# Performance work log

Hardware: AMD Instinct MI355X
Metric: run time of the kernel (lower is better)

Reference implementation:

```python
import jax, jax.numpy as jnp
import numpy as np

N = 100000
D = 128
E = 600000


def setup_inputs() -> dict:
    key = jax.random.key(0)
    k = jax.random.split(key, 7)
    x = jax.random.normal(k[0], (N, D), dtype=jnp.float32)
    edge_index = jax.random.randint(k[1], (2, E), 0, N, dtype=jnp.int32)
    edge_weight = jax.random.uniform(k[2], (E,), dtype=jnp.float32)
    # Linear params (torch nn.Linear: y = x @ W.T + b), init scale ~ 1/sqrt(D)
    s = 1.0 / np.sqrt(D)
    W1 = jax.random.uniform(k[3], (D, D), minval=-s, maxval=s, dtype=jnp.float32)
    b1 = jax.random.uniform(k[4], (D,), minval=-s, maxval=s, dtype=jnp.float32)
    W2 = jax.random.uniform(k[5], (D, D), minval=-s, maxval=s, dtype=jnp.float32)
    b2 = jax.random.uniform(k[6], (D,), minval=-s, maxval=s, dtype=jnp.float32)
    return {"x": x, "edge_index": edge_index, "edge_weight": edge_weight,
            "W1": W1, "b1": b1, "W2": W2, "b2": b2}


def reference(x, edge_index, edge_weight, W1, b1, W2, b2):
    row, col = edge_index[0], edge_index[1]
    # gather-weight-scatter: agg[col] += w * x[row]
    msgs = edge_weight[:, None] * x[row]            # [E, D]
    agg = jax.ops.segment_sum(msgs, col, num_segments=x.shape[0])  # [N, D]
    h = (agg + x) @ W1.T + b1 + (agg * x) @ W2.T + b2
    out = jax.nn.leaky_relu(h, negative_slope=0.2)
    # dropout omitted (eval-mode reference)
    return out
```

## Files before the change

### kernel.cpp

```cpp
#include <hip/hip_runtime.h>

#define D 128

typedef __attribute__((ext_vector_type(8))) short short8;
typedef __attribute__((ext_vector_type(4))) float f32x4;

struct OvfE { int dst, row; float w; };

__device__ __forceinline__ unsigned int f2bf(float f) {
  unsigned int u = __float_as_uint(f);
  return (u + 0x7fffu + ((u >> 16) & 1u)) >> 16;
}

__global__ __launch_bounds__(256) void pre_k(
    const float* __restrict__ x, unsigned short* __restrict__ xbf, int n8, int XB,
    const int* __restrict__ ei, const float* __restrict__ ew,
    int* __restrict__ deg, int* __restrict__ ovfcnt,
    int2* __restrict__ slots, OvfE* __restrict__ ovf, int ovfcap,
    int capLog2, int E, int FB,
    const float* __restrict__ W1, const float* __restrict__ b1,
    const float* __restrict__ W2, const float* __restrict__ b2,
    unsigned short* __restrict__ Bpack, float* __restrict__ bsum) {
  int b = blockIdx.x;
  if (b < XB) {
    int tid = b * 256 + threadIdx.x;
    if (tid >= n8) return;
    float4 a = ((const float4*)x)[(size_t)tid * 2];
    float4 c = ((const float4*)x)[(size_t)tid * 2 + 1];
    uint4 o;
    o.x = f2bf(a.x) | (f2bf(a.y) << 16);
    o.y = f2bf(a.z) | (f2bf(a.w) << 16);
    o.z = f2bf(c.x) | (f2bf(c.y) << 16);
    o.w = f2bf(c.z) | (f2bf(c.w) << 16);
    ((uint4*)xbf)[tid] = o;
  } else if (b < XB + FB) {
    int e = (b - XB) * 256 + threadIdx.x;
    if (e >= E) return;
    int c = ei[E + e];
    int p = atomicAdd(&deg[c], 1);
    if (p < (1 << capLog2)) {
      slots[((size_t)c << capLog2) + p] = make_int2(ei[e], __float_as_int(ew[e]));
    } else {
      int oi = atomicAdd(ovfcnt, 1);
      if (oi < ovfcap) { ovf[oi].dst = c; ovf[oi].row = ei[e]; ovf[oi].w = ew[e]; }
    }
  } else {
    int tid = (b - XB - FB) * 256 + threadIdx.x;
    if (tid < 32768) {
      int j = tid & 7;
      int l = (tid >> 3) & 63;
      int ktnt = tid >> 9;
      int kt = ktnt >> 3, nt = ktnt & 7;
      int k = kt * 32 + ((l >> 4) << 3) + j;
      int col = nt * 16 + (l & 15);
      float v = (k < 128) ? W1[col * 128 + k] : W2[col * 128 + (k - 128)];
      Bpack[tid] = (unsigned short)f2bf(v);
    }
    if (tid < 128) bsum[tid] = b1[tid] + b2[tid];
  }
}

__global__ __launch_bounds__(256, 4) void aggfused_k(
    const unsigned short* __restrict__ xbf, const float* __restrict__ x,
    const int* __restrict__ deg, const int2* __restrict__ slots,
    const int* __restrict__ ovfcnt, const OvfE* __restrict__ ovf,
    const unsigned short* __restrict__ Bpack, const float* __restrict__ bsum,
    float* __restrict__ out, int Nn, int capLog2, int usebf) {
  constexpr int ROWB = 528;
  __shared__ __align__(16) unsigned char Us[64 * ROWB];
  const int t = threadIdx.x;
  const int node0 = blockIdx.x * 64;
  const int lane = t & 63, w = t >> 6;
  const int half = lane >> 5, sl = lane & 31;
  const int cap = 1 << capLog2;

  int dall = 0;
  {
    int g = node0 + w * 16 + lane;
    if (lane < 16 && g < Nn) dall = deg[g];
  }
  int ovn = 0;
  if (__any(dall > cap)) ovn = *ovfcnt;

  for (int ii = 0; ii < 8; ++ii) {
    int nodeIdx = ii * 2 + half;
    int g = node0 + w * 16 + nodeIdx;
    int dv = __shfl(dall, nodeIdx);
    f32x4 acc = {0.f, 0.f, 0.f, 0.f};
    if (g < Nn && dv > 0) {
      int d = min(dv, cap);
      const int2* sb = slots + ((size_t)g << capLog2);
      if (usebf) {
        for (int p = 0; p < d; p += 8) {
          int2 e[8];
          #pragma unroll
          for (int q = 0; q < 8; ++q) e[q] = sb[min(p + q, d - 1)];
          uint2 v[8];
          #pragma unroll
          for (int q = 0; q < 8; ++q)
            v[q] = *(const uint2*)(xbf + (size_t)e[q].x * D + sl * 4);
          #pragma unroll
          for (int q = 0; q < 8; ++q) {
            float wt = (p + q < d) ? __int_as_float(e[q].y) : 0.f;
            acc[0] += wt * __uint_as_float(v[q].x << 16);
            acc[1] += wt * __uint_as_float(v[q].x & 0xffff0000u);
            acc[2] += wt * __uint_as_float(v[q].y << 16);
            acc[3] += wt * __uint_as_float(v[q].y & 0xffff0000u);
          }
        }
      } else {
        for (int p = 0; p < d; p += 8) {
          int2 e[8];
          #pragma unroll
          for (int q = 0; q < 8; ++q) e[q] = sb[min(p + q, d - 1)];
          float4 v[8];
          #pragma unroll
          for (int q = 0; q < 8; ++q)
            v[q] = ((const float4*)(x + (size_t)e[q].x * D))[sl];
          #pragma unroll
          for (int q = 0; q < 8; ++q) {
            float wt = (p + q < d) ? __int_as_float(e[q].y) : 0.f;
            acc[0] += wt * v[q].x;
            acc[1] += wt * v[q].y;
            acc[2] += wt * v[q].z;
            acc[3] += wt * v[q].w;
          }
        }
      }
      if (dv > cap) {
        for (int j = 0; j < ovn; ++j) {
          if (ovf[j].dst == g) {
            float wt = ovf[j].w;
            int r = ovf[j].row;
            if (usebf) {
              uint2 v = *(const uint2*)(xbf + (size_t)r * D + sl * 4);
              acc[0] += wt * __uint_as_float(v.x << 16);
              acc[1] += wt * __uint_as_float(v.x & 0xffff0000u);
              acc[2] += wt * __uint_as_float(v.y << 16);
              acc[3] += wt * __uint_as_float(v.y & 0xffff0000u);
            } else {
              float4 v = ((const float4*)(x + (size_t)r * D))[sl];
              acc[0] += wt * v.x; acc[1] += wt * v.y;
              acc[2] += wt * v.z; acc[3] += wt * v.w;
            }
          }
        }
      }
    }
    float4 xr = make_float4(0.f, 0.f, 0.f, 0.f);
    if (g < Nn) xr = ((const float4*)(x + (size_t)g * D))[sl];
    uint2 up, vp;
    up.x = f2bf(acc[0] + xr.x) | (f2bf(acc[1] + xr.y) << 16);
    up.y = f2bf(acc[2] + xr.z) | (f2bf(acc[3] + xr.w) << 16);
    vp.x = f2bf(acc[0] * xr.x) | (f2bf(acc[1] * xr.y) << 16);
    vp.y = f2bf(acc[2] * xr.z) | (f2bf(acc[3] * xr.w) << 16);
    int nrow = w * 16 + nodeIdx;
    *(uint2*)(Us + nrow * ROWB + sl * 8)       = up;
    *(uint2*)(Us + nrow * ROWB + 256 + sl * 8) = vp;
  }
  __syncthreads();

  const int c15 = lane & 15, kq = lane >> 4;

  short8 afr[8];
  const unsigned char* abase = Us + (size_t)(w * 16 + c15) * ROWB + kq * 16;
  #pragma unroll
  for (int kt = 0; kt < 8; ++kt)
    afr[kt] = *(const short8*)(abase + kt * 64);

  f32x4 acc2[8];
  #pragma unroll
  for (int nt = 0; nt < 8; ++nt) acc2[nt] = (f32x4){0.f, 0.f, 0.f, 0.f};

  const short8* bp = (const short8*)Bpack + lane;
  #pragma unroll
  for (int kt = 0; kt < 8; ++kt) {
    #pragma unroll
    for (int nt = 0; nt < 8; ++nt) {
      short8 bfr = bp[(kt * 8 + nt) * 64];
      acc2[nt] = __builtin_amdgcn_mfma_f32_16x16x32_bf16(afr[kt], bfr, acc2[nt], 0, 0, 0);
    }
  }

  float bsv[8];
  #pragma unroll
  for (int nt = 0; nt < 8; ++nt) bsv[nt] = bsum[nt * 16 + c15];

  #pragma unroll
  for (int r = 0; r < 4; ++r) {
    int g = node0 + w * 16 + kq * 4 + r;
    if (g >= Nn) continue;
    float* orow = out + (size_t)g * D + c15;
    #pragma unroll
    for (int nt = 0; nt < 8; ++nt) {
      float h = acc2[nt][r] + bsv[nt];
      orow[nt * 16] = h > 0.f ? h : 0.2f * h;
    }
  }
}

extern "C" void kernel_launch(void* const* d_in, const int* in_sizes, int n_in,
                              void* d_out, int out_size, void* d_ws, size_t ws_size,
                              hipStream_t stream) {
  const float* x  = (const float*)d_in[0];
  const int*   ei = (const int*)d_in[1];
  const float* ew = (const float*)d_in[2];
  const float* W1 = (const float*)d_in[3];
  const float* b1 = (const float*)d_in[4];
  const float* W2 = (const float*)d_in[5];
  const float* b2 = (const float*)d_in[6];
  float* out = (float*)d_out;

  const int Nn = in_sizes[0] / D;
  const int E  = in_sizes[2];
  const int n8 = Nn * D / 8;

  auto al = [](size_t v) { return (v + 255) & ~(size_t)255; };
  const int ovfcap = 65536;
  const size_t degB   = al((size_t)(Nn + 1) * 4);
  const size_t ovfB   = al((size_t)ovfcap * sizeof(OvfE));
  const size_t BpackB = 65536;
  const size_t bsB    = 512;
  const size_t xbfB   = al((size_t)Nn * D * 2);
  const size_t fixedB = degB + ovfB + BpackB + bsB;

  int capLog2, usebf;
  if      (ws_size >= fixedB + (((size_t)Nn << 5) * 8) + xbfB) { capLog2 = 5; usebf = 1; }
  else if (ws_size >= fixedB + (((size_t)Nn << 4) * 8) + xbfB) { capLog2 = 4; usebf = 1; }
  else if (ws_size >= fixedB + (((size_t)Nn << 4) * 8))        { capLog2 = 4; usebf = 0; }
  else                                                         { capLog2 = 3; usebf = 0; }
  const size_t slotsB = al(((size_t)Nn << capLog2) * 8);

  char* base = (char*)d_ws;
  int*  deg    = (int*)base;                      base += degB;
  OvfE* ovf    = (OvfE*)base;                     base += ovfB;
  unsigned short* Bpack = (unsigned short*)base;  base += BpackB;
  float* bs    = (float*)base;                    base += bsB;
  int2* slots  = (int2*)base;                     base += slotsB;
  unsigned short* xbf = (unsigned short*)base;

  hipMemsetAsync(deg, 0, (size_t)(Nn + 1) * 4, stream);

  const int XB = usebf ? (n8 + 255) / 256 : 0;
  const int FB = (E + 255) / 256;
  pre_k<<<XB + FB + 128, 256, 0, stream>>>(
      x, xbf, n8, XB, ei, ew, deg, deg + Nn, slots, ovf, ovfcap,
      capLog2, E, FB, W1, b1, W2, b2, Bpack, bs);

  aggfused_k<<<(Nn + 63) / 64, 256, 0, stream>>>(
      usebf ? xbf : (const unsigned short*)nullptr, x, deg, slots,
      deg + Nn, ovf, Bpack, bs, out, Nn, capLog2, usebf);
}
```

Measured before the change: 218.8 us.

## Gather 16-byte bf16 rows for four nodes per wave and prefetch edge slots

Remaps the aggregation so 16 lanes each load 8 bf16 values (16 bytes) per neighbor row, letting one wave handle four nodes at once instead of two. The first eight edge slots of all four nodes are loaded up front, so more gathers are in flight and the serial per-node load latency is hidden. Each wave writes and reads only its own LDS rows, so the block-wide barrier is removed. The fp32 fallback path is also dropped, which means low-workspace configurations now assume bf16 space exists, and register pressure rises from the larger prefetch arrays.

```diff
diff --git a/kernel.cpp b/kernel.cpp
--- a/kernel.cpp
+++ b/kernel.cpp
@@ -10,6 +10,12 @@
 __device__ __forceinline__ unsigned int f2bf(float f) {
   unsigned int u = __float_as_uint(f);
   return (u + 0x7fffu + ((u >> 16) & 1u)) >> 16;
+}
+__device__ __forceinline__ float bfl(unsigned int u) {
+  return __uint_as_float(u << 16);
+}
+__device__ __forceinline__ float bfh(unsigned int u) {
+  return __uint_as_float(u & 0xffff0000u);
 }
 
 __global__ __launch_bounds__(256) void pre_k(
@@ -65,13 +71,13 @@
     const int* __restrict__ deg, const int2* __restrict__ slots,
     const int* __restrict__ ovfcnt, const OvfE* __restrict__ ovf,
     const unsigned short* __restrict__ Bpack, const float* __restrict__ bsum,
-    float* __restrict__ out, int Nn, int capLog2, int usebf) {
+    float* __restrict__ out, int Nn, int capLog2) {
   constexpr int ROWB = 528;
   __shared__ __align__(16) unsigned char Us[64 * ROWB];
   const int t = threadIdx.x;
   const int node0 = blockIdx.x * 64;
   const int lane = t & 63, w = t >> 6;
-  const int half = lane >> 5, sl = lane & 31;
+  const int q = lane >> 4, ql = lane & 15;
   const int cap = 1 << capLog2;
 
   int dall = 0;
@@ -82,83 +88,95 @@
   int ovn = 0;
   if (__any(dall > cap)) ovn = *ovfcnt;
 
-  for (int ii = 0; ii < 8; ++ii) {
-    int nodeIdx = ii * 2 + half;
+  int dv[4], gg[4];
+  const int2* sb[4];
+  #pragma unroll
+  for (int ii = 0; ii < 4; ++ii) {
+    int nodeIdx = ii * 4 + q;
     int g = node0 + w * 16 + nodeIdx;
-    int dv = __shfl(dall, nodeIdx);
-    f32x4 acc = {0.f, 0.f, 0.f, 0.f};
-    if (g < Nn && dv > 0) {
-      int d = min(dv, cap);
-      const int2* sb = slots + ((size_t)g << capLog2);
-      if (usebf) {
-        for (int p = 0; p < d; p += 8) {
-          int2 e[8];
-          #pragma unroll
-          for (int q = 0; q < 8; ++q) e[q] = sb[min(p + q, d - 1)];
-          uint2 v[8];
-          #pragma unroll
-          for (int q = 0; q < 8; ++q)
-            v[q] = *(const uint2*)(xbf + (size_t)e[q].x * D + sl * 4);
-          #pragma unroll
-          for (int q = 0; q < 8; ++q) {
-            float wt = (p + q < d) ? __int_as_float(e[q].y) : 0.f;
-            acc[0] += wt * __uint_as_float(v[q].x << 16);
-            acc[1] += wt * __uint_as_float(v[q].x & 0xffff0000u);
-            acc[2] += wt * __uint_as_float(v[q].y << 16);
-            acc[3] += wt * __uint_as_float(v[q].y & 0xffff0000u);
-          }
+    dv[ii] = __shfl(dall, nodeIdx);
+    gg[ii] = g;
+    sb[ii] = slots + ((size_t)min(g, Nn - 1) << capLog2);
+  }
+
+  int2 e0[4][8];
+  #pragma unroll
+  for (int ii = 0; ii < 4; ++ii) {
+    int dm = max(dv[ii] - 1, 0);
+    #pragma unroll
+    for (int j = 0; j < 8; ++j) e0[ii][j] = sb[ii][min(j, dm)];
+  }
+
+  #pragma unroll
+  for (int ii = 0; ii < 4; ++ii) {
+    float acc[8] = {0.f, 0.f, 0.f, 0.f, 0.f, 0.f, 0.f, 0.f};
+    {
+      uint4 v[8];
+      #pragma unroll
+      for (int j = 0; j < 8; ++j) {
+        int r = min(max(e0[ii][j].x, 0), Nn - 1);
+        v[j] = *(const uint4*)(xbf + (size_t)r * D + ql * 8);
+      }
+      #pragma unroll
+      for (int j = 0; j < 8; ++j) {
+        float wt = (j < dv[ii]) ? __int_as_float(e0[ii][j].y) : 0.f;
+        acc[0] += wt * bfl(v[j].x); acc[1] += wt * bfh(v[j].x);
+        acc[2] += wt * bfl(v[j].y); acc[3] += wt * bfh(v[j].y);
+        acc[4] += wt * bfl(v[j].z); acc[5] += wt * bfh(v[j].z);
+        acc[6] += wt * bfl(v[j].w); acc[7] += wt * bfh(v[j].w);
+      }
+    }
+    for (int p = 8; p < dv[ii]; p += 8) {
+      int2 e2[8];
+      #pragma unroll
+      for (int j = 0; j < 8; ++j) e2[j] = sb[ii][min(p + j, dv[ii] - 1)];
+      uint4 v2[8];
+      #pragma unroll
+      for (int j = 0; j < 8; ++j) {
+        int r = min(max(e2[j].x, 0), Nn - 1);
+        v2[j] = *(const uint4*)(xbf + (size_t)r * D + ql * 8);
+      }
+      #pragma unroll
+      for (int j = 0; j < 8; ++j) {
+        float wt = (p + j < dv[ii]) ? __int_as_float(e2[j].y) : 0.f;
+        acc[0] += wt * bfl(v2[j].x); acc[1] += wt * bfh(v2[j].x);
+        acc[2] += wt * bfl(v2[j].y); acc[3] += wt * bfh(v2[j].y);
+        acc[4] += wt * bfl(v2[j].z); acc[5] += wt * bfh(v2[j].z);
+        acc[6] += wt * bfl(v2[j].w); acc[7] += wt * bfh(v2[j].w);
+      }
+    }
+    if (dv[ii] > cap) {
+      for (int jj = 0; jj < ovn; ++jj) {
+        if (ovf[jj].dst == gg[ii]) {
+          float wt = ovf[jj].w;
+          int r = ovf[jj].row;
+          uint4 v = *(const uint4*)(xbf + (size_t)r * D + ql * 8);
+          acc[0] += wt * bfl(v.x); acc[1] += wt * bfh(v.x);
+          acc[2] += wt * bfl(v.y); acc[3] += wt * bfh(v.y);
+          acc[4] += wt * bfl(v.z); acc[5] += wt * bfh(v.z);
+          acc[6] += wt * bfl(v.w); acc[7] += wt * bfh(v.w);
         }
-      } else {
-        for (int p = 0; p < d; p += 8) {
-          int2 e[8];
-          #pragma unroll
-          for (int q = 0; q < 8; ++q) e[q] = sb[min(p + q, d - 1)];
-          float4 v[8];
-          #pragma unroll
-          for (int q = 0; q < 8; ++q)
-            v[q] = ((const float4*)(x + (size_t)e[q].x * D))[sl];
-          #pragma unroll
-          for (int q = 0; q < 8; ++q) {
-            float wt = (p + q < d) ? __int_as_float(e[q].y) : 0.f;
-            acc[0] += wt * v[q].x;
-            acc[1] += wt * v[q].y;
-            acc[2] += wt * v[q].z;
-            acc[3] += wt * v[q].w;
-          }
-        }
-      }
-      if (dv > cap) {
-        for (int j = 0; j < ovn; ++j) {
-          if (ovf[j].dst == g) {
-            float wt = ovf[j].w;
-            int r = ovf[j].row;
-            if (usebf) {
-              uint2 v = *(const uint2*)(xbf + (size_t)r * D + sl * 4);
-              acc[0] += wt * __uint_as_float(v.x << 16);
-              acc[1] += wt * __uint_as_float(v.x & 0xffff0000u);
-              acc[2] += wt * __uint_as_float(v.y << 16);
-              acc[3] += wt * __uint_as_float(v.y & 0xffff0000u);
-            } else {
-              float4 v = ((const float4*)(x + (size_t)r * D))[sl];
-              acc[0] += wt * v.x; acc[1] += wt * v.y;
-              acc[2] += wt * v.z; acc[3] += wt * v.w;
-            }
-          }
-        }
-      }
-    }
-    float4 xr = make_float4(0.f, 0.f, 0.f, 0.f);
-    if (g < Nn) xr = ((const float4*)(x + (size_t)g * D))[sl];
-    uint2 up, vp;
-    up.x = f2bf(acc[0] + xr.x) | (f2bf(acc[1] + xr.y) << 16);
-    up.y = f2bf(acc[2] + xr.z) | (f2bf(acc[3] + xr.w) << 16);
-    vp.x = f2bf(acc[0] * xr.x) | (f2bf(acc[1] * xr.y) << 16);
-    vp.y = f2bf(acc[2] * xr.z) | (f2bf(acc[3] * xr.w) << 16);
-    int nrow = w * 16 + nodeIdx;
-    *(uint2*)(Us + nrow * ROWB + sl * 8)       = up;
-    *(uint2*)(Us + nrow * ROWB + 256 + sl * 8) = vp;
-  }
-  __syncthreads();
+      }
+    }
+    float4 xa = make_float4(0.f, 0.f, 0.f, 0.f), xb = xa;
+    if (gg[ii] < Nn) {
+      const float4* xr = (const float4*)(x + (size_t)gg[ii] * D);
+      xa = xr[ql * 2];
+      xb = xr[ql * 2 + 1];
+    }
+    uint4 up, vp;
+    up.x = f2bf(acc[0] + xa.x) | (f2bf(acc[1] + xa.y) << 16);
+    up.y = f2bf(acc[2] + xa.z) | (f2bf(acc[3] + xa.w) << 16);
+    up.z = f2bf(acc[4] + xb.x) | (f2bf(acc[5] + xb.y) << 16);
+    up.w = f2bf(acc[6] + xb.z) | (f2bf(acc[7] + xb.w) << 16);
+    vp.x = f2bf(acc[0] * xa.x) | (f2bf(acc[1] * xa.y) << 16);
+    vp.y = f2bf(acc[2] * xa.z) | (f2bf(acc[3] * xa.w) << 16);
+    vp.z = f2bf(acc[4] * xb.x) | (f2bf(acc[5] * xb.y) << 16);
+    vp.w = f2bf(acc[6] * xb.z) | (f2bf(acc[7] * xb.w) << 16);
+    int nrow = w * 16 + ii * 4 + q;
+    *(uint4*)(Us + nrow * ROWB + ql * 16)       = up;
+    *(uint4*)(Us + nrow * ROWB + 256 + ql * 16) = vp;
+  }
 
   const int c15 = lane & 15, kq = lane >> 4;
 
@@ -224,11 +242,10 @@
   const size_t xbfB   = al((size_t)Nn * D * 2);
   const size_t fixedB = degB + ovfB + BpackB + bsB;
 
-  int capLog2, usebf;
-  if      (ws_size >= fixedB + (((size_t)Nn << 5) * 8) + xbfB) { capLog2 = 5; usebf = 1; }
-  else if (ws_size >= fixedB + (((size_t)Nn << 4) * 8) + xbfB) { capLog2 = 4; usebf = 1; }
-  else if (ws_size >= fixedB + (((size_t)Nn << 4) * 8))        { capLog2 = 4; usebf = 0; }
-  else                                                         { capLog2 = 3; usebf = 0; }
+  int capLog2;
+  if      (ws_size >= fixedB + (((size_t)Nn << 5) * 8) + xbfB) capLog2 = 5;
+  else if (ws_size >= fixedB + (((size_t)Nn << 4) * 8) + xbfB) capLog2 = 4;
+  else                                                         capLog2 = 3;
   const size_t slotsB = al(((size_t)Nn << capLog2) * 8);
 
   char* base = (char*)d_ws;
@@ -241,13 +258,12 @@
 
   hipMemsetAsync(deg, 0, (size_t)(Nn + 1) * 4, stream);
 
-  const int XB = usebf ? (n8 + 255) / 256 : 0;
+  const int XB = (n8 + 255) / 256;
   const int FB = (E + 255) / 256;
   pre_k<<<XB + FB + 128, 256, 0, stream>>>(
       x, xbf, n8, XB, ei, ew, deg, deg + Nn, slots, ovf, ovfcap,
       capLog2, E, FB, W1, b1, W2, b2, Bpack, bs);
 
   aggfused_k<<<(Nn + 63) / 64, 256, 0, stream>>>(
-      usebf ? xbf : (const unsigned short*)nullptr, x, deg, slots,
-      deg + Nn, ovf, Bpack, bs, out, Nn, capLog2, usebf);
-}
+      xbf, x, deg, slots, deg + Nn, ovf, Bpack, bs, out, Nn, capLog2);
+}
```

Result: faster. 205.6 us (-6.0%).
